# Performance work log

Measured on AMD Instinct MI355X. Metric: run time of the kernel, lower is better.

## Reference

```python
import jax, jax.numpy as jnp
import numpy as np

VOCAB = 1024
D = 1024  # predictor_dim
B = 32
U = 512
NULL_INDEX = 0


def setup_inputs() -> dict:
    key = jax.random.key(0)
    ks = jax.random.split(key, 9)
    s = 1.0 / np.sqrt(D)
    return {
        "y": jax.random.randint(ks[0], (B, U), 0, VOCAB, dtype=jnp.int32),
        "embed_table": jax.random.normal(ks[1], (VOCAB, D), jnp.float32) * s,
        "Wx": jax.random.normal(ks[2], (D, 3 * D), jnp.float32) * s,  # input kernel [z|r|h]
        "Wh": jax.random.normal(ks[3], (D, 3 * D), jnp.float32) * s,  # recurrent kernel [z|r|h]
        "bx": jnp.zeros((3 * D,), jnp.float32),  # input bias (reset_after=True)
        "bh": jnp.zeros((3 * D,), jnp.float32),  # recurrent bias (reset_after=True)
        "Wd": jax.random.normal(ks[4], (D, D), jnp.float32) * s,
        "bd": jnp.zeros((D,), jnp.float32),
        "h0": jax.random.normal(ks[5], (D,), jnp.float32),  # self.initial_state
    }


def _gru_scan(tokens, embed_table, Wx, Wh, bx, bh, h0_b):
    # tokens: [B, T] int; returns hidden states [B, T, D]
    x = embed_table[tokens]                       # [B, T, D]
    # Precompute all input projections outside the recurrence (one big GEMM)
    xp = jnp.einsum("btd,de->bte", x, Wx) + bx    # [B, T, 3D]
    xp = jnp.moveaxis(xp, 1, 0)                   # [T, B, 3D]

    def step(h, xp_t):
        hp = h @ Wh + bh                          # [B, 3D], reset_after=True
        xz, xr, xh = jnp.split(xp_t, 3, axis=-1)
        hz, hr, hh = jnp.split(hp, 3, axis=-1)
        z = jax.nn.sigmoid(xz + hz)
        r = jax.nn.sigmoid(xr + hr)
        hcand = jnp.tanh(xh + r * hh)
        h_new = z * h + (1.0 - z) * hcand
        return h_new, h_new

    _, hs = jax.lax.scan(step, h0_b, xp)          # hs: [T, B, D]
    return jnp.moveaxis(hs, 0, 1)                 # [B, T, D]


def reference(y, embed_table, Wx, Wh, bx, bh, Wd, bd, h0):
    Bn = y.shape[0]
    start = jnp.full((Bn, 1), NULL_INDEX, dtype=y.dtype)
    tokens = jnp.concatenate([start, y], axis=1)  # [B, U+1]
    h0_b = jnp.broadcast_to(h0, (Bn, D))
    hs = _gru_scan(tokens, embed_table, Wx, Wh, bx, bh, h0_b)  # [B, U+1, D]
    outs = jnp.einsum("btd,de->bte", hs, Wd) + bd
    return outs
```

## Files before the change

kernel.cpp:

```cpp
#include <hip/hip_runtime.h>
#include <hip/hip_bf16.h>
#include <cstdint>

typedef __bf16 bf16;
typedef __bf16 bf16x8 __attribute__((ext_vector_type(8)));
typedef float  f32x4  __attribute__((ext_vector_type(4)));
typedef uint32_t u32x4 __attribute__((ext_vector_type(4)));

#define D_DIM   1024
#define ND      3072
#define B_SZ    32
#define U_SZ    512
#define T_SZ    513
#define M_REAL  (B_SZ * T_SZ)
#define WXS_LD  1032
#define A_LD    1032

#define AGENT __HIP_MEMORY_SCOPE_AGENT

__device__ __forceinline__ f32x4 mfma16(bf16x8 a, bf16x8 b, f32x4 c) {
    return __builtin_amdgcn_mfma_f32_16x16x32_bf16(a, b, c, 0, 0, 0);
}

struct bfpair { bf16x8 hi, lo; };

__device__ __forceinline__ bfpair split8(const float* p) {
    f32x4 a = *(const f32x4*)p;
    f32x4 b = *(const f32x4*)(p + 4);
    bfpair r;
#pragma unroll
    for (int j = 0; j < 4; ++j) {
        r.hi[j] = (bf16)a[j];
        r.lo[j] = (bf16)(a[j] - (float)r.hi[j]);
        r.hi[4 + j] = (bf16)b[j];
        r.lo[4 + j] = (bf16)(b[j] - (float)r.hi[4 + j]);
    }
    return r;
}

__device__ __forceinline__ bf16x8 cvt8(const float* p) {
    f32x4 a = *(const f32x4*)p;
    f32x4 b = *(const f32x4*)(p + 4);
    bf16x8 r;
#pragma unroll
    for (int j = 0; j < 4; ++j) { r[j] = (bf16)a[j]; r[4 + j] = (bf16)b[j]; }
    return r;
}

__device__ __forceinline__ bfpair unpack8(const uint32_t* p) {
    u32x4 a = *(const u32x4*)p;
    u32x4 b = *(const u32x4*)(p + 4);
    union { uint32_t u[4]; bf16x8 v; } H, L;
    H.u[0] = __builtin_amdgcn_perm(a.y, a.x, 0x05040100u);
    H.u[1] = __builtin_amdgcn_perm(a.w, a.z, 0x05040100u);
    H.u[2] = __builtin_amdgcn_perm(b.y, b.x, 0x05040100u);
    H.u[3] = __builtin_amdgcn_perm(b.w, b.z, 0x05040100u);
    L.u[0] = __builtin_amdgcn_perm(a.y, a.x, 0x07060302u);
    L.u[1] = __builtin_amdgcn_perm(a.w, a.z, 0x07060302u);
    L.u[2] = __builtin_amdgcn_perm(b.y, b.x, 0x07060302u);
    L.u[3] = __builtin_amdgcn_perm(b.w, b.z, 0x07060302u);
    bfpair r; r.hi = H.v; r.lo = L.v;
    return r;
}

__global__ void transpose_split(const float* __restrict__ in,
                                bf16* __restrict__ out_hi, bf16* __restrict__ out_lo,
                                int R, int C) {
    __shared__ float tile[32][33];
    const int c0 = blockIdx.x * 32, r0 = blockIdx.y * 32;
    const int tx = threadIdx.x, ty = threadIdx.y;
    for (int i = 0; i < 32; i += 8)
        tile[ty + i][tx] = in[(size_t)(r0 + ty + i) * C + c0 + tx];
    __syncthreads();
    for (int i = 0; i < 32; i += 8) {
        const float v  = tile[tx][ty + i];
        const bf16  hi = (bf16)v;
        out_hi[(size_t)(c0 + ty + i) * R + r0 + tx] = hi;
        out_lo[(size_t)(c0 + ty + i) * R + r0 + tx] = (bf16)(v - (float)hi);
    }
}

__global__ __launch_bounds__(256, 1)
void gru_scan(const float* __restrict__ Wx,    const float* __restrict__ Wh,
              const float* __restrict__ bx,    const float* __restrict__ bh,
              const float* __restrict__ h0,    const float* __restrict__ embed,
              const int* __restrict__ y,       uint32_t* __restrict__ ghs,
              int* __restrict__ flags)
{
    __shared__ __align__(16) bf16 WxS[48 * WXS_LD];
    __shared__ float hpx[48 * 17];
    __shared__ float xpx[2][48 * 17];
    __shared__ float bhs[48], bxs[48];

    const int tid  = threadIdx.x;
    const int wave = tid >> 6, lane = tid & 63;
    const int quad = lane >> 4, l15 = lane & 15;
    const int mhalf = blockIdx.x & 1;
    const int n0 = (blockIdx.x >> 1) * 16;
    int* slots = flags;
    int* go    = flags + 512;

    for (int idx = tid; idx < 3 * 1024 * 16; idx += 256) {
        const int cl = idx & 15;
        const int k  = (idx >> 4) & 1023;
        const int g  = idx >> 14;
        WxS[(g * 16 + cl) * WXS_LD + k] = (bf16)Wx[(size_t)k * ND + g * D_DIM + n0 + cl];
    }
    if (tid < 48) {
        bhs[tid] = bh[(tid >> 4) * D_DIM + n0 + (tid & 15)];
        bxs[tid] = bx[(tid >> 4) * D_DIM + n0 + (tid & 15)];
    }

    bf16x8 breg[32];
    if (wave < 3) {
#pragma unroll
        for (int ks = 0; ks < 32; ++ks) {
            bf16x8 v;
#pragma unroll
            for (int j = 0; j < 8; ++j)
                v[j] = (bf16)Wh[(size_t)(ks * 32 + quad * 8 + j) * ND
                                + wave * D_DIM + n0 + l15];
            breg[ks] = v;
        }
    }

    const int gml = tid >> 4, nl = tid & 15;
    const int gb  = mhalf * 16 + gml;
    const int gn  = n0 + nl;
    float hold = h0[gn];
    uint32_t pkjunk = 0;

    __syncthreads();

    if (wave == 3) {
        const float* xrow = embed + quad * 8;
        f32x4 ax0 = {}, ax1 = {}, ax2 = {};
#pragma unroll
        for (int ks = 0; ks < 32; ++ks) {
            bf16x8 xa = cvt8(xrow + ks * 32);
            bf16x8 w0 = *(const bf16x8*)(WxS + (l15)      * WXS_LD + ks * 32 + quad * 8);
            bf16x8 w1 = *(const bf16x8*)(WxS + (16 + l15) * WXS_LD + ks * 32 + quad * 8);
            bf16x8 w2 = *(const bf16x8*)(WxS + (32 + l15) * WXS_LD + ks * 32 + quad * 8);
            ax0 = mfma16(xa, w0, ax0);
            ax1 = mfma16(xa, w1, ax1);
            ax2 = mfma16(xa, w2, ax2);
        }
#pragma unroll
        for (int i = 0; i < 4; ++i) {
            xpx[0][(quad * 4 + i) * 17 + l15]      = ax0[i];
            xpx[0][(16 + quad * 4 + i) * 17 + l15] = ax1[i];
            xpx[0][(32 + quad * 4 + i) * 17 + l15] = ax2[i];
        }
    }

    for (int t = 0; t < T_SZ; ++t) {
        if (wave < 3) {
            f32x4 a0 = {}, a1 = {};
            if (t == 0) {
                const float* hrow = h0 + quad * 8;
#pragma unroll
                for (int ks = 0; ks < 32; ++ks) {
                    bfpair h8 = split8(hrow + ks * 32);
                    a0 = mfma16(h8.hi, breg[ks], a0);
                    a1 = mfma16(h8.lo, breg[ks], a1);
                }
            } else {
                const uint32_t* hrow = ghs
                    + ((size_t)(mhalf * 16 + l15) * T_SZ + (t - 1)) * D_DIM + quad * 8;
#pragma unroll
                for (int ks = 0; ks < 32; ++ks) {
                    bfpair h8 = unpack8(hrow + ks * 32);
                    a0 = mfma16(h8.hi, breg[ks], a0);
                    a1 = mfma16(h8.lo, breg[ks], a1);
                }
            }
            a0 = a0 + a1;
#pragma unroll
            for (int i = 0; i < 4; ++i)
                hpx[(wave * 16 + quad * 4 + i) * 17 + l15] = a0[i];
        }

        if (wave == 3 && t < U_SZ) {
            const int tok = y[(mhalf * 16 + l15) * U_SZ + t] & 1023;
            const float* xrow = embed + (size_t)tok * D_DIM + quad * 8;
            const int p = (t + 1) & 1;
            f32x4 ax0 = {}, ax1 = {}, ax2 = {};
#pragma unroll
            for (int ks = 0; ks < 32; ++ks) {
                bf16x8 xa = cvt8(xrow + ks * 32);
                bf16x8 w0 = *(const bf16x8*)(WxS + (l15)      * WXS_LD + ks * 32 + quad * 8);
                bf16x8 w1 = *(const bf16x8*)(WxS + (16 + l15) * WXS_LD + ks * 32 + quad * 8);
                bf16x8 w2 = *(const bf16x8*)(WxS + (32 + l15) * WXS_LD + ks * 32 + quad * 8);
                ax0 = mfma16(xa, w0, ax0);
                ax1 = mfma16(xa, w1, ax1);
                ax2 = mfma16(xa, w2, ax2);
            }
#pragma unroll
            for (int i = 0; i < 4; ++i) {
                xpx[p][(quad * 4 + i) * 17 + l15]      = ax0[i];
                xpx[p][(16 + quad * 4 + i) * 17 + l15] = ax1[i];
                xpx[p][(32 + quad * 4 + i) * 17 + l15] = ax2[i];
            }
        }
        __syncthreads();

        {
            const int p = t & 1;
            const float xz = xpx[p][(gml)      * 17 + nl] + bxs[nl];
            const float xr = xpx[p][(16 + gml) * 17 + nl] + bxs[16 + nl];
            const float xh = xpx[p][(32 + gml) * 17 + nl] + bxs[32 + nl];
            const float hz = hpx[(gml)      * 17 + nl] + bhs[nl];
            const float hr = hpx[(16 + gml) * 17 + nl] + bhs[16 + nl];
            const float hh = hpx[(32 + gml) * 17 + nl] + bhs[32 + nl];
            const float z  = 1.f / (1.f + __expf(-(xz + hz)));
            const float r  = 1.f / (1.f + __expf(-(xr + hr)));
            const float pa = xh + r * hh;
            const float hc = 1.f - 2.f / (__expf(2.f * pa) + 1.f);
            const float hn = z * hold + (1.f - z) * hc;
            hold = hn;
            union { uint16_t u[2]; uint32_t w; } pk;
            const bf16 hi = (bf16)hn;
            const bf16 lo = (bf16)(hn - (float)hi);
            pk.u[0] = __builtin_bit_cast(uint16_t, hi);
            pk.u[1] = __builtin_bit_cast(uint16_t, lo);
            uint32_t old = __hip_atomic_exchange(
                ghs + ((size_t)gb * T_SZ + t) * D_DIM + gn, pk.w,
                __ATOMIC_RELAXED, AGENT);
            pkjunk ^= old;
        }

        if (t + 1 < T_SZ) {
            __syncthreads();
            const int tv = t + 1;
            if (blockIdx.x == 0) {
                if (wave == 0) {
                    int ok;
                    do {
                        const int s1 = __hip_atomic_load(slots + lane * 4,
                                                         __ATOMIC_RELAXED, AGENT);
                        const int s2 = __hip_atomic_load(slots + (lane + 64) * 4,
                                                         __ATOMIC_RELAXED, AGENT);
                        ok = (lane == 0 || s1 >= tv) && (s2 >= tv);
                    } while (!__all(ok));
                    if (lane < 8)
                        __hip_atomic_store(go + lane * 16, tv,
                                           __ATOMIC_RELAXED, AGENT);
                }
            } else {
                if (tid == 0) {
                    __hip_atomic_store(slots + blockIdx.x * 4, tv,
                                       __ATOMIC_RELAXED, AGENT);
                    while (__hip_atomic_load(go + (blockIdx.x & 7) * 16,
                                             __ATOMIC_RELAXED, AGENT) < tv) {}
                }
            }
            __syncthreads();
        }
    }

    if (pkjunk == 0xDEADBEEFu) flags[1023] = 1;
}

__global__ __launch_bounds__(256, 1)
void gemm_rows_inplace(float* __restrict__ C,
                       const bf16* __restrict__ WdTh, const bf16* __restrict__ WdTl,
                       const float* __restrict__ bd)
{
    __shared__ __align__(16) bf16 Ah[32 * A_LD];
    __shared__ __align__(16) bf16 Al[32 * A_LD];
    const int tid  = threadIdx.x;
    const int wave = tid >> 6, lane = tid & 63;
    const int quad = lane >> 4, l15 = lane & 15;
    const size_t r0 = (size_t)blockIdx.x * 32;
    const uint32_t* Cw = (const uint32_t*)C;

    for (int idx = tid; idx < 32 * 128; idx += 256) {
        const int r = idx >> 7, ch = idx & 127;
        bfpair p = unpack8(Cw + (r0 + r) * D_DIM + ch * 8);
        *(bf16x8*)(Ah + r * A_LD + ch * 8) = p.hi;
        *(bf16x8*)(Al + r * A_LD + ch * 8) = p.lo;
    }
    __syncthreads();

    f32x4 acc[2][16] = {};
    const int nbase = wave * 256;
    for (int ks = 0; ks < 32; ++ks) {
        bf16x8 a0h = *(const bf16x8*)(Ah + (l15)      * A_LD + ks * 32 + quad * 8);
        bf16x8 a0l = *(const bf16x8*)(Al + (l15)      * A_LD + ks * 32 + quad * 8);
        bf16x8 a1h = *(const bf16x8*)(Ah + (16 + l15) * A_LD + ks * 32 + quad * 8);
        bf16x8 a1l = *(const bf16x8*)(Al + (16 + l15) * A_LD + ks * 32 + quad * 8);
#pragma unroll
        for (int nt = 0; nt < 16; ++nt) {
            const size_t boff = (size_t)(nbase + nt * 16 + l15) * D_DIM + ks * 32 + quad * 8;
            bf16x8 bhv = *(const bf16x8*)(WdTh + boff);
            bf16x8 blv = *(const bf16x8*)(WdTl + boff);
            acc[0][nt] = mfma16(a0h, bhv, acc[0][nt]);
            acc[0][nt] = mfma16(a0l, bhv, acc[0][nt]);
            acc[0][nt] = mfma16(a0h, blv, acc[0][nt]);
            acc[1][nt] = mfma16(a1h, bhv, acc[1][nt]);
            acc[1][nt] = mfma16(a1l, bhv, acc[1][nt]);
            acc[1][nt] = mfma16(a1h, blv, acc[1][nt]);
        }
    }

#pragma unroll
    for (int nt = 0; nt < 16; ++nt) {
        const int col = nbase + nt * 16 + l15;
        const float bvl = bd[col];
#pragma unroll
        for (int mt = 0; mt < 2; ++mt)
#pragma unroll
            for (int i = 0; i < 4; ++i)
                C[(r0 + mt * 16 + quad * 4 + i) * D_DIM + col] =
                    acc[mt][nt][i] + bvl;
    }
}

extern "C" void kernel_launch(void* const* d_in, const int* in_sizes, int n_in,
                              void* d_out, int out_size, void* d_ws, size_t ws_size,
                              hipStream_t stream) {
    (void)in_sizes; (void)n_in; (void)out_size; (void)ws_size;
    const int*   y     = (const int*)  d_in[0];
    const float* embed = (const float*)d_in[1];
    const float* Wx    = (const float*)d_in[2];
    const float* Wh    = (const float*)d_in[3];
    const float* bx    = (const float*)d_in[4];
    const float* bh    = (const float*)d_in[5];
    const float* Wd    = (const float*)d_in[6];
    const float* bd    = (const float*)d_in[7];
    const float* h0    = (const float*)d_in[8];
    float* out = (float*)d_out;

    bf16* WdTh = (bf16*)d_ws;
    bf16* WdTl = WdTh + (size_t)D_DIM * D_DIM;
    int* flags = (int*)((char*)d_ws + (size_t)D_DIM * D_DIM * 4);

    hipMemsetAsync(flags, 0, 8192, stream);

    transpose_split<<<dim3(D_DIM / 32, D_DIM / 32), dim3(32, 8), 0, stream>>>(
        Wd, WdTh, WdTl, D_DIM, D_DIM);

    gru_scan<<<128, 256, 0, stream>>>(Wx, Wh, bx, bh, h0, embed, y,
                                      (uint32_t*)out, flags);

    gemm_rows_inplace<<<M_REAL / 32, 256, 0, stream>>>(out, WdTh, WdTl, bd);
}
```

Baseline: 7.573 ms.

## Halve scan grid, compute gates in MFMA waves, use all-to-all flag barrier

The GRU scan now runs on 64 blocks instead of 128. Each block covers 16 output columns for all 32 batch rows. Two waves each hold the z, r and h recurrent weights in registers and apply the gate nonlinearities directly on their MFMA accumulators, which removes the hpx shared-memory round trip and one __syncthreads per step. The centralized block-0 barrier with go flags is replaced by a decentralized barrier: each block publishes its step counter and every block polls all 64 slots. This cuts per-step synchronization latency, but each MFMA wave now issues three times as many MFMAs and holds three times the weight registers (96 bf16x8 per lane), so register pressure may rise.

```diff
diff --git a/kernel.cpp b/kernel.cpp
--- a/kernel.cpp
+++ b/kernel.cpp
@@ -15,6 +15,7 @@
 #define M_REAL  (B_SZ * T_SZ)
 #define WXS_LD  1032
 #define A_LD    1032
+#define XP_LD   20
 
 #define AGENT __HIP_MEMORY_SCOPE_AGENT
 
@@ -88,17 +89,14 @@
               int* __restrict__ flags)
 {
     __shared__ __align__(16) bf16 WxS[48 * WXS_LD];
-    __shared__ float hpx[48 * 17];
-    __shared__ float xpx[2][48 * 17];
-    __shared__ float bhs[48], bxs[48];
+    __shared__ __align__(16) float xpx[2][96 * XP_LD];
+    __shared__ __align__(16) float bxs[3][16], bhs[3][16];
 
     const int tid  = threadIdx.x;
     const int wave = tid >> 6, lane = tid & 63;
     const int quad = lane >> 4, l15 = lane & 15;
-    const int mhalf = blockIdx.x & 1;
-    const int n0 = (blockIdx.x >> 1) * 16;
+    const int n0 = blockIdx.x * 16;
     int* slots = flags;
-    int* go    = flags + 512;
 
     for (int idx = tid; idx < 3 * 1024 * 16; idx += 256) {
         const int cl = idx & 15;
@@ -107,32 +105,33 @@
         WxS[(g * 16 + cl) * WXS_LD + k] = (bf16)Wx[(size_t)k * ND + g * D_DIM + n0 + cl];
     }
     if (tid < 48) {
-        bhs[tid] = bh[(tid >> 4) * D_DIM + n0 + (tid & 15)];
-        bxs[tid] = bx[(tid >> 4) * D_DIM + n0 + (tid & 15)];
-    }
-
-    bf16x8 breg[32];
-    if (wave < 3) {
+        bxs[tid >> 4][tid & 15] = bx[(tid >> 4) * D_DIM + n0 + (tid & 15)];
+        bhs[tid >> 4][tid & 15] = bh[(tid >> 4) * D_DIM + n0 + (tid & 15)];
+    }
+
+    bf16x8 bregZ[32], bregR[32], bregH[32];
+    if (wave < 2) {
 #pragma unroll
         for (int ks = 0; ks < 32; ++ks) {
-            bf16x8 v;
-#pragma unroll
-            for (int j = 0; j < 8; ++j)
-                v[j] = (bf16)Wh[(size_t)(ks * 32 + quad * 8 + j) * ND
-                                + wave * D_DIM + n0 + l15];
-            breg[ks] = v;
-        }
-    }
-
-    const int gml = tid >> 4, nl = tid & 15;
-    const int gb  = mhalf * 16 + gml;
-    const int gn  = n0 + nl;
-    float hold = h0[gn];
-    uint32_t pkjunk = 0;
+            bf16x8 vz, vr, vh;
+#pragma unroll
+            for (int j = 0; j < 8; ++j) {
+                const size_t krow = (size_t)(ks * 32 + quad * 8 + j) * ND + n0 + l15;
+                vz[j] = (bf16)Wh[krow];
+                vr[j] = (bf16)Wh[krow + D_DIM];
+                vh[j] = (bf16)Wh[krow + 2 * D_DIM];
+            }
+            bregZ[ks] = vz; bregR[ks] = vr; bregH[ks] = vh;
+        }
+    }
+
+    const int batch = (wave & 1) * 16 + l15;
+    f32x4 holdv = *(const f32x4*)(h0 + n0 + quad * 4);
+    unsigned long long junk = 0;
 
     __syncthreads();
 
-    if (wave == 3) {
+    if (wave >= 2) {
         const float* xrow = embed + quad * 8;
         f32x4 ax0 = {}, ax1 = {}, ax2 = {};
 #pragma unroll
@@ -141,47 +140,83 @@
             bf16x8 w0 = *(const bf16x8*)(WxS + (l15)      * WXS_LD + ks * 32 + quad * 8);
             bf16x8 w1 = *(const bf16x8*)(WxS + (16 + l15) * WXS_LD + ks * 32 + quad * 8);
             bf16x8 w2 = *(const bf16x8*)(WxS + (32 + l15) * WXS_LD + ks * 32 + quad * 8);
-            ax0 = mfma16(xa, w0, ax0);
-            ax1 = mfma16(xa, w1, ax1);
-            ax2 = mfma16(xa, w2, ax2);
-        }
-#pragma unroll
-        for (int i = 0; i < 4; ++i) {
-            xpx[0][(quad * 4 + i) * 17 + l15]      = ax0[i];
-            xpx[0][(16 + quad * 4 + i) * 17 + l15] = ax1[i];
-            xpx[0][(32 + quad * 4 + i) * 17 + l15] = ax2[i];
-        }
-    }
+            ax0 = mfma16(w0, xa, ax0);
+            ax1 = mfma16(w1, xa, ax1);
+            ax2 = mfma16(w2, xa, ax2);
+        }
+        *(f32x4*)(xpx[0] + (batch)      * XP_LD + quad * 4) = ax0;
+        *(f32x4*)(xpx[0] + (32 + batch) * XP_LD + quad * 4) = ax1;
+        *(f32x4*)(xpx[0] + (64 + batch) * XP_LD + quad * 4) = ax2;
+    }
+    __syncthreads();
 
     for (int t = 0; t < T_SZ; ++t) {
-        if (wave < 3) {
-            f32x4 a0 = {}, a1 = {};
+        if (wave < 2) {
+            f32x4 azh = {}, azl = {}, arh = {}, arl = {}, ahh = {}, ahl = {};
             if (t == 0) {
                 const float* hrow = h0 + quad * 8;
 #pragma unroll
                 for (int ks = 0; ks < 32; ++ks) {
                     bfpair h8 = split8(hrow + ks * 32);
-                    a0 = mfma16(h8.hi, breg[ks], a0);
-                    a1 = mfma16(h8.lo, breg[ks], a1);
+                    azh = mfma16(bregZ[ks], h8.hi, azh);
+                    azl = mfma16(bregZ[ks], h8.lo, azl);
+                    arh = mfma16(bregR[ks], h8.hi, arh);
+                    arl = mfma16(bregR[ks], h8.lo, arl);
+                    ahh = mfma16(bregH[ks], h8.hi, ahh);
+                    ahl = mfma16(bregH[ks], h8.lo, ahl);
                 }
             } else {
                 const uint32_t* hrow = ghs
-                    + ((size_t)(mhalf * 16 + l15) * T_SZ + (t - 1)) * D_DIM + quad * 8;
+                    + ((size_t)batch * T_SZ + (t - 1)) * D_DIM + quad * 8;
 #pragma unroll
                 for (int ks = 0; ks < 32; ++ks) {
                     bfpair h8 = unpack8(hrow + ks * 32);
-                    a0 = mfma16(h8.hi, breg[ks], a0);
-                    a1 = mfma16(h8.lo, breg[ks], a1);
+                    azh = mfma16(bregZ[ks], h8.hi, azh);
+                    azl = mfma16(bregZ[ks], h8.lo, azl);
+                    arh = mfma16(bregR[ks], h8.hi, arh);
+                    arl = mfma16(bregR[ks], h8.lo, arl);
+                    ahh = mfma16(bregH[ks], h8.hi, ahh);
+                    ahl = mfma16(bregH[ks], h8.lo, ahl);
                 }
             }
-            a0 = a0 + a1;
-#pragma unroll
-            for (int i = 0; i < 4; ++i)
-                hpx[(wave * 16 + quad * 4 + i) * 17 + l15] = a0[i];
-        }
-
-        if (wave == 3 && t < U_SZ) {
-            const int tok = y[(mhalf * 16 + l15) * U_SZ + t] & 1023;
+
+            const int p = t & 1;
+            const f32x4 xz = *(const f32x4*)(xpx[p] + (batch)      * XP_LD + quad * 4);
+            const f32x4 xr = *(const f32x4*)(xpx[p] + (32 + batch) * XP_LD + quad * 4);
+            const f32x4 xh = *(const f32x4*)(xpx[p] + (64 + batch) * XP_LD + quad * 4);
+            const f32x4 bxz = *(const f32x4*)(&bxs[0][quad * 4]);
+            const f32x4 bxr = *(const f32x4*)(&bxs[1][quad * 4]);
+            const f32x4 bxh = *(const f32x4*)(&bxs[2][quad * 4]);
+            const f32x4 bhz = *(const f32x4*)(&bhs[0][quad * 4]);
+            const f32x4 bhr = *(const f32x4*)(&bhs[1][quad * 4]);
+            const f32x4 bhh = *(const f32x4*)(&bhs[2][quad * 4]);
+            uint32_t pk[4];
+#pragma unroll
+            for (int i = 0; i < 4; ++i) {
+                const float hz  = azh[i] + azl[i] + bhz[i];
+                const float hr  = arh[i] + arl[i] + bhr[i];
+                const float hhv = ahh[i] + ahl[i] + bhh[i];
+                const float z  = 1.f / (1.f + __expf(-(xz[i] + bxz[i] + hz)));
+                const float r  = 1.f / (1.f + __expf(-(xr[i] + bxr[i] + hr)));
+                const float pa = xh[i] + bxh[i] + r * hhv;
+                const float hc = 1.f - 2.f / (__expf(2.f * pa) + 1.f);
+                const float hn = z * holdv[i] + (1.f - z) * hc;
+                holdv[i] = hn;
+                const bf16 hi = (bf16)hn;
+                const bf16 lo = (bf16)(hn - (float)hi);
+                pk[i] = (uint32_t)__builtin_bit_cast(uint16_t, hi)
+                      | ((uint32_t)__builtin_bit_cast(uint16_t, lo) << 16);
+            }
+            const unsigned long long e0 = (unsigned long long)pk[0]
+                                        | ((unsigned long long)pk[1] << 32);
+            const unsigned long long e1 = (unsigned long long)pk[2]
+                                        | ((unsigned long long)pk[3] << 32);
+            unsigned long long* dst = (unsigned long long*)
+                (ghs + ((size_t)batch * T_SZ + t) * D_DIM + n0 + quad * 4);
+            junk ^= __hip_atomic_exchange(dst,     e0, __ATOMIC_RELAXED, AGENT);
+            junk ^= __hip_atomic_exchange(dst + 1, e1, __ATOMIC_RELAXED, AGENT);
+        } else if (t < U_SZ) {
+            const int tok = y[batch * U_SZ + t] & 1023;
             const float* xrow = embed + (size_t)tok * D_DIM + quad * 8;
             const int p = (t + 1) & 1;
             f32x4 ax0 = {}, ax1 = {}, ax2 = {};
@@ -191,74 +226,33 @@
                 bf16x8 w0 = *(const bf16x8*)(WxS + (l15)      * WXS_LD + ks * 32 + quad * 8);
                 bf16x8 w1 = *(const bf16x8*)(WxS + (16 + l15) * WXS_LD + ks * 32 + quad * 8);
                 bf16x8 w2 = *(const bf16x8*)(WxS + (32 + l15) * WXS_LD + ks * 32 + quad * 8);
-                ax0 = mfma16(xa, w0, ax0);
-                ax1 = mfma16(xa, w1, ax1);
-                ax2 = mfma16(xa, w2, ax2);
-            }
-#pragma unroll
-            for (int i = 0; i < 4; ++i) {
-                xpx[p][(quad * 4 + i) * 17 + l15]      = ax0[i];
-                xpx[p][(16 + quad * 4 + i) * 17 + l15] = ax1[i];
-                xpx[p][(32 + quad * 4 + i) * 17 + l15] = ax2[i];
-            }
-        }
+                ax0 = mfma16(w0, xa, ax0);
+                ax1 = mfma16(w1, xa, ax1);
+                ax2 = mfma16(w2, xa, ax2);
+            }
+            *(f32x4*)(xpx[p] + (batch)      * XP_LD + quad * 4) = ax0;
+            *(f32x4*)(xpx[p] + (32 + batch) * XP_LD + quad * 4) = ax1;
+            *(f32x4*)(xpx[p] + (64 + batch) * XP_LD + quad * 4) = ax2;
+        }
+
         __syncthreads();
 
-        {
-            const int p = t & 1;
-            const float xz = xpx[p][(gml)      * 17 + nl] + bxs[nl];
-            const float xr = xpx[p][(16 + gml) * 17 + nl] + bxs[16 + nl];
-            const float xh = xpx[p][(32 + gml) * 17 + nl] + bxs[32 + nl];
-            const float hz = hpx[(gml)      * 17 + nl] + bhs[nl];
-            const float hr = hpx[(16 + gml) * 17 + nl] + bhs[16 + nl];
-            const float hh = hpx[(32 + gml) * 17 + nl] + bhs[32 + nl];
-            const float z  = 1.f / (1.f + __expf(-(xz + hz)));
-            const float r  = 1.f / (1.f + __expf(-(xr + hr)));
-            const float pa = xh + r * hh;
-            const float hc = 1.f - 2.f / (__expf(2.f * pa) + 1.f);
-            const float hn = z * hold + (1.f - z) * hc;
-            hold = hn;
-            union { uint16_t u[2]; uint32_t w; } pk;
-            const bf16 hi = (bf16)hn;
-            const bf16 lo = (bf16)(hn - (float)hi);
-            pk.u[0] = __builtin_bit_cast(uint16_t, hi);
-            pk.u[1] = __builtin_bit_cast(uint16_t, lo);
-            uint32_t old = __hip_atomic_exchange(
-                ghs + ((size_t)gb * T_SZ + t) * D_DIM + gn, pk.w,
-                __ATOMIC_RELAXED, AGENT);
-            pkjunk ^= old;
-        }
-
         if (t + 1 < T_SZ) {
-            __syncthreads();
             const int tv = t + 1;
-            if (blockIdx.x == 0) {
-                if (wave == 0) {
-                    int ok;
-                    do {
-                        const int s1 = __hip_atomic_load(slots + lane * 4,
-                                                         __ATOMIC_RELAXED, AGENT);
-                        const int s2 = __hip_atomic_load(slots + (lane + 64) * 4,
-                                                         __ATOMIC_RELAXED, AGENT);
-                        ok = (lane == 0 || s1 >= tv) && (s2 >= tv);
-                    } while (!__all(ok));
-                    if (lane < 8)
-                        __hip_atomic_store(go + lane * 16, tv,
-                                           __ATOMIC_RELAXED, AGENT);
-                }
-            } else {
-                if (tid == 0) {
-                    __hip_atomic_store(slots + blockIdx.x * 4, tv,
-                                       __ATOMIC_RELAXED, AGENT);
-                    while (__hip_atomic_load(go + (blockIdx.x & 7) * 16,
-                                             __ATOMIC_RELAXED, AGENT) < tv) {}
-                }
-            }
-            __syncthreads();
-        }
-    }
-
-    if (pkjunk == 0xDEADBEEFu) flags[1023] = 1;
+            if (tid == 0)
+                __hip_atomic_store(slots + (blockIdx.x << 4), tv,
+                                   __ATOMIC_RELAXED, AGENT);
+            if (wave < 2) {
+                int s;
+                do {
+                    s = __hip_atomic_load(slots + (lane << 4),
+                                          __ATOMIC_RELAXED, AGENT);
+                } while (__any(s < tv));
+            }
+        }
+    }
+
+    if (junk == 0xDEADBEEFDEADBEEFull) flags[1023] = 1;
 }
 
 __global__ __launch_bounds__(256, 1)
@@ -340,8 +334,8 @@
     transpose_split<<<dim3(D_DIM / 32, D_DIM / 32), dim3(32, 8), 0, stream>>>(
         Wd, WdTh, WdTl, D_DIM, D_DIM);
 
-    gru_scan<<<128, 256, 0, stream>>>(Wx, Wh, bx, bh, h0, embed, y,
-                                      (uint32_t*)out, flags);
+    gru_scan<<<64, 256, 0, stream>>>(Wx, Wh, bx, bh, h0, embed, y,
+                                     (uint32_t*)out, flags);
 
     gemm_rows_inplace<<<M_REAL / 32, 256, 0, stream>>>(out, WdTh, WdTl, bd);
 }
```

Result: slower. 8.286 ms (+9.4%).

## Fuse output projection GEMM into scan kernel as concurrently running consumer blocks

Applied to the files above, without the earlier changes.

The separate output GEMM kernel is merged into the GRU scan kernel. The launch grows to 256 blocks: the first 128 run the recurrence as before, and the other 128 act as consumers. Each consumer waits on the per-step `go` flag until its 32-row chunk is final and no longer read by the recurrence, then runs the projection in place. Shared memory is overlaid with a union. The aim is to hide the output GEMM behind the latency-bound scan, at the cost of extra memory contention during the scan. It also requires all 256 blocks to be co-resident, or the spin-waits deadlock.

```diff
diff --git a/kernel.cpp b/kernel.cpp
--- a/kernel.cpp
+++ b/kernel.cpp
@@ -13,6 +13,7 @@
 #define U_SZ    512
 #define T_SZ    513
 #define M_REAL  (B_SZ * T_SZ)
+#define NCHUNK  (M_REAL / 32)
 #define WXS_LD  1032
 #define A_LD    1032
 
@@ -80,239 +81,258 @@
     }
 }
 
+struct ScanS {
+    bf16  WxS[48 * WXS_LD];
+    float hpx[48 * 17];
+    float xpx[2][48 * 17];
+    float bhs[48], bxs[48];
+};
+struct GemmS {
+    bf16 Ah[32 * A_LD];
+    bf16 Al[32 * A_LD];
+};
+union SMemU { ScanS s; GemmS g; };
+
 __global__ __launch_bounds__(256, 1)
 void gru_scan(const float* __restrict__ Wx,    const float* __restrict__ Wh,
               const float* __restrict__ bx,    const float* __restrict__ bh,
               const float* __restrict__ h0,    const float* __restrict__ embed,
               const int* __restrict__ y,       uint32_t* __restrict__ ghs,
-              int* __restrict__ flags)
+              int* __restrict__ flags,
+              const bf16* __restrict__ WdTh,   const bf16* __restrict__ WdTl,
+              const float* __restrict__ bd)
 {
-    __shared__ __align__(16) bf16 WxS[48 * WXS_LD];
-    __shared__ float hpx[48 * 17];
-    __shared__ float xpx[2][48 * 17];
-    __shared__ float bhs[48], bxs[48];
+    __shared__ __align__(16) SMemU su;
 
     const int tid  = threadIdx.x;
     const int wave = tid >> 6, lane = tid & 63;
     const int quad = lane >> 4, l15 = lane & 15;
-    const int mhalf = blockIdx.x & 1;
-    const int n0 = (blockIdx.x >> 1) * 16;
     int* slots = flags;
     int* go    = flags + 512;
 
-    for (int idx = tid; idx < 3 * 1024 * 16; idx += 256) {
-        const int cl = idx & 15;
-        const int k  = (idx >> 4) & 1023;
-        const int g  = idx >> 14;
-        WxS[(g * 16 + cl) * WXS_LD + k] = (bf16)Wx[(size_t)k * ND + g * D_DIM + n0 + cl];
-    }
-    if (tid < 48) {
-        bhs[tid] = bh[(tid >> 4) * D_DIM + n0 + (tid & 15)];
-        bxs[tid] = bx[(tid >> 4) * D_DIM + n0 + (tid & 15)];
-    }
-
-    bf16x8 breg[32];
-    if (wave < 3) {
-#pragma unroll
-        for (int ks = 0; ks < 32; ++ks) {
-            bf16x8 v;
-#pragma unroll
-            for (int j = 0; j < 8; ++j)
-                v[j] = (bf16)Wh[(size_t)(ks * 32 + quad * 8 + j) * ND
-                                + wave * D_DIM + n0 + l15];
-            breg[ks] = v;
-        }
-    }
-
-    const int gml = tid >> 4, nl = tid & 15;
-    const int gb  = mhalf * 16 + gml;
-    const int gn  = n0 + nl;
-    float hold = h0[gn];
-    uint32_t pkjunk = 0;
-
-    __syncthreads();
-
-    if (wave == 3) {
-        const float* xrow = embed + quad * 8;
-        f32x4 ax0 = {}, ax1 = {}, ax2 = {};
-#pragma unroll
-        for (int ks = 0; ks < 32; ++ks) {
-            bf16x8 xa = cvt8(xrow + ks * 32);
-            bf16x8 w0 = *(const bf16x8*)(WxS + (l15)      * WXS_LD + ks * 32 + quad * 8);
-            bf16x8 w1 = *(const bf16x8*)(WxS + (16 + l15) * WXS_LD + ks * 32 + quad * 8);
-            bf16x8 w2 = *(const bf16x8*)(WxS + (32 + l15) * WXS_LD + ks * 32 + quad * 8);
-            ax0 = mfma16(xa, w0, ax0);
-            ax1 = mfma16(xa, w1, ax1);
-            ax2 = mfma16(xa, w2, ax2);
-        }
-#pragma unroll
-        for (int i = 0; i < 4; ++i) {
-            xpx[0][(quad * 4 + i) * 17 + l15]      = ax0[i];
-            xpx[0][(16 + quad * 4 + i) * 17 + l15] = ax1[i];
-            xpx[0][(32 + quad * 4 + i) * 17 + l15] = ax2[i];
-        }
-    }
-
-    for (int t = 0; t < T_SZ; ++t) {
+    if (blockIdx.x < 128) {
+        const int mhalf = blockIdx.x & 1;
+        const int n0 = (blockIdx.x >> 1) * 16;
+
+        for (int idx = tid; idx < 3 * 1024 * 16; idx += 256) {
+            const int cl = idx & 15;
+            const int k  = (idx >> 4) & 1023;
+            const int g  = idx >> 14;
+            su.s.WxS[(g * 16 + cl) * WXS_LD + k] =
+                (bf16)Wx[(size_t)k * ND + g * D_DIM + n0 + cl];
+        }
+        if (tid < 48) {
+            su.s.bhs[tid] = bh[(tid >> 4) * D_DIM + n0 + (tid & 15)];
+            su.s.bxs[tid] = bx[(tid >> 4) * D_DIM + n0 + (tid & 15)];
+        }
+
+        bf16x8 breg[32];
         if (wave < 3) {
-            f32x4 a0 = {}, a1 = {};
-            if (t == 0) {
-                const float* hrow = h0 + quad * 8;
-#pragma unroll
-                for (int ks = 0; ks < 32; ++ks) {
-                    bfpair h8 = split8(hrow + ks * 32);
-                    a0 = mfma16(h8.hi, breg[ks], a0);
-                    a1 = mfma16(h8.lo, breg[ks], a1);
-                }
-            } else {
-                const uint32_t* hrow = ghs
-                    + ((size_t)(mhalf * 16 + l15) * T_SZ + (t - 1)) * D_DIM + quad * 8;
-#pragma unroll
-                for (int ks = 0; ks < 32; ++ks) {
-                    bfpair h8 = unpack8(hrow + ks * 32);
-                    a0 = mfma16(h8.hi, breg[ks], a0);
-                    a1 = mfma16(h8.lo, breg[ks], a1);
-                }
-            }
-            a0 = a0 + a1;
-#pragma unroll
-            for (int i = 0; i < 4; ++i)
-                hpx[(wave * 16 + quad * 4 + i) * 17 + l15] = a0[i];
-        }
-
-        if (wave == 3 && t < U_SZ) {
-            const int tok = y[(mhalf * 16 + l15) * U_SZ + t] & 1023;
-            const float* xrow = embed + (size_t)tok * D_DIM + quad * 8;
-            const int p = (t + 1) & 1;
+#pragma unroll
+            for (int ks = 0; ks < 32; ++ks) {
+                bf16x8 v;
+#pragma unroll
+                for (int j = 0; j < 8; ++j)
+                    v[j] = (bf16)Wh[(size_t)(ks * 32 + quad * 8 + j) * ND
+                                    + wave * D_DIM + n0 + l15];
+                breg[ks] = v;
+            }
+        }
+
+        const int gml = tid >> 4, nl = tid & 15;
+        const int gb  = mhalf * 16 + gml;
+        const int gn  = n0 + nl;
+        float hold = h0[gn];
+        uint32_t pkjunk = 0;
+
+        __syncthreads();
+
+        if (wave == 3) {
+            const float* xrow = embed + quad * 8;
             f32x4 ax0 = {}, ax1 = {}, ax2 = {};
 #pragma unroll
             for (int ks = 0; ks < 32; ++ks) {
                 bf16x8 xa = cvt8(xrow + ks * 32);
-                bf16x8 w0 = *(const bf16x8*)(WxS + (l15)      * WXS_LD + ks * 32 + quad * 8);
-                bf16x8 w1 = *(const bf16x8*)(WxS + (16 + l15) * WXS_LD + ks * 32 + quad * 8);
-                bf16x8 w2 = *(const bf16x8*)(WxS + (32 + l15) * WXS_LD + ks * 32 + quad * 8);
+                bf16x8 w0 = *(const bf16x8*)(su.s.WxS + (l15)      * WXS_LD + ks * 32 + quad * 8);
+                bf16x8 w1 = *(const bf16x8*)(su.s.WxS + (16 + l15) * WXS_LD + ks * 32 + quad * 8);
+                bf16x8 w2 = *(const bf16x8*)(su.s.WxS + (32 + l15) * WXS_LD + ks * 32 + quad * 8);
                 ax0 = mfma16(xa, w0, ax0);
                 ax1 = mfma16(xa, w1, ax1);
                 ax2 = mfma16(xa, w2, ax2);
             }
 #pragma unroll
             for (int i = 0; i < 4; ++i) {
-                xpx[p][(quad * 4 + i) * 17 + l15]      = ax0[i];
-                xpx[p][(16 + quad * 4 + i) * 17 + l15] = ax1[i];
-                xpx[p][(32 + quad * 4 + i) * 17 + l15] = ax2[i];
-            }
-        }
-        __syncthreads();
-
-        {
-            const int p = t & 1;
-            const float xz = xpx[p][(gml)      * 17 + nl] + bxs[nl];
-            const float xr = xpx[p][(16 + gml) * 17 + nl] + bxs[16 + nl];
-            const float xh = xpx[p][(32 + gml) * 17 + nl] + bxs[32 + nl];
-            const float hz = hpx[(gml)      * 17 + nl] + bhs[nl];
-            const float hr = hpx[(16 + gml) * 17 + nl] + bhs[16 + nl];
-            const float hh = hpx[(32 + gml) * 17 + nl] + bhs[32 + nl];
-            const float z  = 1.f / (1.f + __expf(-(xz + hz)));
-            const float r  = 1.f / (1.f + __expf(-(xr + hr)));
-            const float pa = xh + r * hh;
-            const float hc = 1.f - 2.f / (__expf(2.f * pa) + 1.f);
-            const float hn = z * hold + (1.f - z) * hc;
-            hold = hn;
-            union { uint16_t u[2]; uint32_t w; } pk;
-            const bf16 hi = (bf16)hn;
-            const bf16 lo = (bf16)(hn - (float)hi);
-            pk.u[0] = __builtin_bit_cast(uint16_t, hi);
-            pk.u[1] = __builtin_bit_cast(uint16_t, lo);
-            uint32_t old = __hip_atomic_exchange(
-                ghs + ((size_t)gb * T_SZ + t) * D_DIM + gn, pk.w,
-                __ATOMIC_RELAXED, AGENT);
-            pkjunk ^= old;
-        }
-
-        if (t + 1 < T_SZ) {
+                su.s.xpx[0][(quad * 4 + i) * 17 + l15]      = ax0[i];
+                su.s.xpx[0][(16 + quad * 4 + i) * 17 + l15] = ax1[i];
+                su.s.xpx[0][(32 + quad * 4 + i) * 17 + l15] = ax2[i];
+            }
+        }
+
+        for (int t = 0; t < T_SZ; ++t) {
+            if (wave < 3) {
+                f32x4 a0 = {}, a1 = {};
+                if (t == 0) {
+                    const float* hrow = h0 + quad * 8;
+#pragma unroll
+                    for (int ks = 0; ks < 32; ++ks) {
+                        bfpair h8 = split8(hrow + ks * 32);
+                        a0 = mfma16(h8.hi, breg[ks], a0);
+                        a1 = mfma16(h8.lo, breg[ks], a1);
+                    }
+                } else {
+                    const uint32_t* hrow = ghs
+                        + ((size_t)(mhalf * 16 + l15) * T_SZ + (t - 1)) * D_DIM + quad * 8;
+#pragma unroll
+                    for (int ks = 0; ks < 32; ++ks) {
+                        bfpair h8 = unpack8(hrow + ks * 32);
+                        a0 = mfma16(h8.hi, breg[ks], a0);
+                        a1 = mfma16(h8.lo, breg[ks], a1);
+                    }
+                }
+                a0 = a0 + a1;
+#pragma unroll
+                for (int i = 0; i < 4; ++i)
+                    su.s.hpx[(wave * 16 + quad * 4 + i) * 17 + l15] = a0[i];
+            }
+
+            if (wave == 3 && t < U_SZ) {
+                const int tok = y[(mhalf * 16 + l15) * U_SZ + t] & 1023;
+                const float* xrow = embed + (size_t)tok * D_DIM + quad * 8;
+                const int p = (t + 1) & 1;
+                f32x4 ax0 = {}, ax1 = {}, ax2 = {};
+#pragma unroll
+                for (int ks = 0; ks < 32; ++ks) {
+                    bf16x8 xa = cvt8(xrow + ks * 32);
+                    bf16x8 w0 = *(const bf16x8*)(su.s.WxS + (l15)      * WXS_LD + ks * 32 + quad * 8);
+                    bf16x8 w1 = *(const bf16x8*)(su.s.WxS + (16 + l15) * WXS_LD + ks * 32 + quad * 8);
+                    bf16x8 w2 = *(const bf16x8*)(su.s.WxS + (32 + l15) * WXS_LD + ks * 32 + quad * 8);
+                    ax0 = mfma16(xa, w0, ax0);
+                    ax1 = mfma16(xa, w1, ax1);
+                    ax2 = mfma16(xa, w2, ax2);
+                }
+#pragma unroll
+                for (int i = 0; i < 4; ++i) {
+                    su.s.xpx[p][(quad * 4 + i) * 17 + l15]      = ax0[i];
+                    su.s.xpx[p][(16 + quad * 4 + i) * 17 + l15] = ax1[i];
+                    su.s.xpx[p][(32 + quad * 4 + i) * 17 + l15] = ax2[i];
+                }
+            }
             __syncthreads();
-            const int tv = t + 1;
-            if (blockIdx.x == 0) {
-                if (wave == 0) {
-                    int ok;
-                    do {
-                        const int s1 = __hip_atomic_load(slots + lane * 4,
-                                                         __ATOMIC_RELAXED, AGENT);
-                        const int s2 = __hip_atomic_load(slots + (lane + 64) * 4,
-                                                         __ATOMIC_RELAXED, AGENT);
-                        ok = (lane == 0 || s1 >= tv) && (s2 >= tv);
-                    } while (!__all(ok));
-                    if (lane < 8)
-                        __hip_atomic_store(go + lane * 16, tv,
+
+            {
+                const int p = t & 1;
+                const float xz = su.s.xpx[p][(gml)      * 17 + nl] + su.s.bxs[nl];
+                const float xr = su.s.xpx[p][(16 + gml) * 17 + nl] + su.s.bxs[16 + nl];
+                const float xh = su.s.xpx[p][(32 + gml) * 17 + nl] + su.s.bxs[32 + nl];
+                const float hz = su.s.hpx[(gml)      * 17 + nl] + su.s.bhs[nl];
+                const float hr = su.s.hpx[(16 + gml) * 17 + nl] + su.s.bhs[16 + nl];
+                const float hh = su.s.hpx[(32 + gml) * 17 + nl] + su.s.bhs[32 + nl];
+                const float z  = 1.f / (1.f + __expf(-(xz + hz)));
+                const float r  = 1.f / (1.f + __expf(-(xr + hr)));
+                const float pa = xh + r * hh;
+                const float hc = 1.f - 2.f / (__expf(2.f * pa) + 1.f);
+                const float hn = z * hold + (1.f - z) * hc;
+                hold = hn;
+                union { uint16_t u[2]; uint32_t w; } pk;
+                const bf16 hi = (bf16)hn;
+                const bf16 lo = (bf16)(hn - (float)hi);
+                pk.u[0] = __builtin_bit_cast(uint16_t, hi);
+                pk.u[1] = __builtin_bit_cast(uint16_t, lo);
+                uint32_t old = __hip_atomic_exchange(
+                    ghs + ((size_t)gb * T_SZ + t) * D_DIM + gn, pk.w,
+                    __ATOMIC_RELAXED, AGENT);
+                pkjunk ^= old;
+            }
+
+            {
+                __syncthreads();
+                const int tv = t + 1;
+                if (blockIdx.x == 0) {
+                    if (wave == 0) {
+                        int ok;
+                        do {
+                            const int s1 = __hip_atomic_load(slots + lane * 4,
+                                                             __ATOMIC_RELAXED, AGENT);
+                            const int s2 = __hip_atomic_load(slots + (lane + 64) * 4,
+                                                             __ATOMIC_RELAXED, AGENT);
+                            ok = (lane == 0 || s1 >= tv) && (s2 >= tv);
+                        } while (!__all(ok));
+                        if (lane < 8)
+                            __hip_atomic_store(go + lane * 16, tv,
+                                               __ATOMIC_RELAXED, AGENT);
+                    }
+                } else {
+                    if (tid == 0) {
+                        __hip_atomic_store(slots + blockIdx.x * 4, tv,
                                            __ATOMIC_RELAXED, AGENT);
-                }
-            } else {
-                if (tid == 0) {
-                    __hip_atomic_store(slots + blockIdx.x * 4, tv,
-                                       __ATOMIC_RELAXED, AGENT);
-                    while (__hip_atomic_load(go + (blockIdx.x & 7) * 16,
-                                             __ATOMIC_RELAXED, AGENT) < tv) {}
-                }
+                        while (__hip_atomic_load(go + (blockIdx.x & 7) * 16,
+                                                 __ATOMIC_RELAXED, AGENT) < tv) {}
+                    }
+                }
+                __syncthreads();
+            }
+        }
+
+        if (pkjunk == 0xDEADBEEFu) flags[1023] = 1;
+
+    } else {
+        const uint32_t* Cw = (const uint32_t*)ghs;
+        float* Cf = (float*)ghs;
+
+        for (int c = (int)blockIdx.x - 128; c < NCHUNK; c += 128) {
+            const int t0   = (c * 32) % T_SZ;
+            const int tmax = (t0 + 31 <= T_SZ - 1) ? (t0 + 31) : (T_SZ - 1);
+            int need = tmax + 2; if (need > T_SZ) need = T_SZ;
+
+            if (tid == 0) {
+                while (__hip_atomic_load(go + (c & 7) * 16,
+                                         __ATOMIC_RELAXED, AGENT) < need)
+                    __builtin_amdgcn_s_sleep(4);
             }
             __syncthreads();
-        }
-    }
-
-    if (pkjunk == 0xDEADBEEFu) flags[1023] = 1;
-}
-
-__global__ __launch_bounds__(256, 1)
-void gemm_rows_inplace(float* __restrict__ C,
-                       const bf16* __restrict__ WdTh, const bf16* __restrict__ WdTl,
-                       const float* __restrict__ bd)
-{
-    __shared__ __align__(16) bf16 Ah[32 * A_LD];
-    __shared__ __align__(16) bf16 Al[32 * A_LD];
-    const int tid  = threadIdx.x;
-    const int wave = tid >> 6, lane = tid & 63;
-    const int quad = lane >> 4, l15 = lane & 15;
-    const size_t r0 = (size_t)blockIdx.x * 32;
-    const uint32_t* Cw = (const uint32_t*)C;
-
-    for (int idx = tid; idx < 32 * 128; idx += 256) {
-        const int r = idx >> 7, ch = idx & 127;
-        bfpair p = unpack8(Cw + (r0 + r) * D_DIM + ch * 8);
-        *(bf16x8*)(Ah + r * A_LD + ch * 8) = p.hi;
-        *(bf16x8*)(Al + r * A_LD + ch * 8) = p.lo;
-    }
-    __syncthreads();
-
-    f32x4 acc[2][16] = {};
-    const int nbase = wave * 256;
-    for (int ks = 0; ks < 32; ++ks) {
-        bf16x8 a0h = *(const bf16x8*)(Ah + (l15)      * A_LD + ks * 32 + quad * 8);
-        bf16x8 a0l = *(const bf16x8*)(Al + (l15)      * A_LD + ks * 32 + quad * 8);
-        bf16x8 a1h = *(const bf16x8*)(Ah + (16 + l15) * A_LD + ks * 32 + quad * 8);
-        bf16x8 a1l = *(const bf16x8*)(Al + (16 + l15) * A_LD + ks * 32 + quad * 8);
-#pragma unroll
-        for (int nt = 0; nt < 16; ++nt) {
-            const size_t boff = (size_t)(nbase + nt * 16 + l15) * D_DIM + ks * 32 + quad * 8;
-            bf16x8 bhv = *(const bf16x8*)(WdTh + boff);
-            bf16x8 blv = *(const bf16x8*)(WdTl + boff);
-            acc[0][nt] = mfma16(a0h, bhv, acc[0][nt]);
-            acc[0][nt] = mfma16(a0l, bhv, acc[0][nt]);
-            acc[0][nt] = mfma16(a0h, blv, acc[0][nt]);
-            acc[1][nt] = mfma16(a1h, bhv, acc[1][nt]);
-            acc[1][nt] = mfma16(a1l, bhv, acc[1][nt]);
-            acc[1][nt] = mfma16(a1h, blv, acc[1][nt]);
-        }
-    }
-
-#pragma unroll
-    for (int nt = 0; nt < 16; ++nt) {
-        const int col = nbase + nt * 16 + l15;
-        const float bvl = bd[col];
-#pragma unroll
-        for (int mt = 0; mt < 2; ++mt)
-#pragma unroll
-            for (int i = 0; i < 4; ++i)
-                C[(r0 + mt * 16 + quad * 4 + i) * D_DIM + col] =
-                    acc[mt][nt][i] + bvl;
+
+            const size_t r0 = (size_t)c * 32;
+            for (int idx = tid; idx < 32 * 128; idx += 256) {
+                const int r = idx >> 7, ch = idx & 127;
+                bfpair p = unpack8(Cw + (r0 + r) * D_DIM + ch * 8);
+                *(bf16x8*)(su.g.Ah + r * A_LD + ch * 8) = p.hi;
+                *(bf16x8*)(su.g.Al + r * A_LD + ch * 8) = p.lo;
+            }
+            __syncthreads();
+
+            f32x4 acc[2][16] = {};
+            const int nbase = wave * 256;
+            for (int ks = 0; ks < 32; ++ks) {
+                bf16x8 a0h = *(const bf16x8*)(su.g.Ah + (l15)      * A_LD + ks * 32 + quad * 8);
+                bf16x8 a0l = *(const bf16x8*)(su.g.Al + (l15)      * A_LD + ks * 32 + quad * 8);
+                bf16x8 a1h = *(const bf16x8*)(su.g.Ah + (16 + l15) * A_LD + ks * 32 + quad * 8);
+                bf16x8 a1l = *(const bf16x8*)(su.g.Al + (16 + l15) * A_LD + ks * 32 + quad * 8);
+#pragma unroll
+                for (int nt = 0; nt < 16; ++nt) {
+                    const size_t boff = (size_t)(nbase + nt * 16 + l15) * D_DIM + ks * 32 + quad * 8;
+                    bf16x8 bhv = *(const bf16x8*)(WdTh + boff);
+                    bf16x8 blv = *(const bf16x8*)(WdTl + boff);
+                    acc[0][nt] = mfma16(a0h, bhv, acc[0][nt]);
+                    acc[0][nt] = mfma16(a0l, bhv, acc[0][nt]);
+                    acc[0][nt] = mfma16(a0h, blv, acc[0][nt]);
+                    acc[1][nt] = mfma16(a1h, bhv, acc[1][nt]);
+                    acc[1][nt] = mfma16(a1l, bhv, acc[1][nt]);
+                    acc[1][nt] = mfma16(a1h, blv, acc[1][nt]);
+                }
+            }
+
+#pragma unroll
+            for (int nt = 0; nt < 16; ++nt) {
+                const int col = nbase + nt * 16 + l15;
+                const float bvl = bd[col];
+#pragma unroll
+                for (int mt = 0; mt < 2; ++mt)
+#pragma unroll
+                    for (int i = 0; i < 4; ++i)
+                        Cf[(r0 + mt * 16 + quad * 4 + i) * D_DIM + col] =
+                            acc[mt][nt][i] + bvl;
+            }
+        }
     }
 }
 
@@ -340,8 +360,6 @@
     transpose_split<<<dim3(D_DIM / 32, D_DIM / 32), dim3(32, 8), 0, stream>>>(
         Wd, WdTh, WdTl, D_DIM, D_DIM);
 
-    gru_scan<<<128, 256, 0, stream>>>(Wx, Wh, bx, bh, h0, embed, y,
-                                      (uint32_t*)out, flags);
-
-    gemm_rows_inplace<<<M_REAL / 32, 256, 0, stream>>>(out, WdTh, WdTl, bd);
-}
+    gru_scan<<<256, 256, 0, stream>>>(Wx, Wh, bx, bh, h0, embed, y,
+                                      (uint32_t*)out, flags, WdTh, WdTl, bd);
+}
```

New measurement: 7.743 ms. +2.2%, slower.
